# Kernel optimization log

Hardware: AMD Instinct MI355X
Metric: run time of the kernel (lower is better)

Reference implementation:

```python
import jax, jax.numpy as jnp
import numpy as np

HIDDEN = 4096
N_HEADS = 32
N_KV_HEADS = 8
HEAD_DIM = 128
ROPE_BASE = 10000.0


def setup_inputs() -> dict:
    key = jax.random.key(0)
    k1, k2, k3, k4, k5 = jax.random.split(key, 5)
    s = 0.02  # init scale for weights
    return {
        "hidden_states": jax.random.normal(k1, (1, 2048, HIDDEN), dtype=jnp.float32),
        "Wq": jax.random.normal(k2, (N_HEADS * HEAD_DIM, HIDDEN), dtype=jnp.float32) * s,
        "Wk": jax.random.normal(k3, (N_KV_HEADS * HEAD_DIM, HIDDEN), dtype=jnp.float32) * s,
        "Wv": jax.random.normal(k4, (N_KV_HEADS * HEAD_DIM, HIDDEN), dtype=jnp.float32) * s,
        "Wo": jax.random.normal(k5, (HIDDEN, HIDDEN), dtype=jnp.float32) * s,
    }


def _rope(x, cos, sin):
    # x: [B, H, T, D]; cos/sin: [T, D/2] -> rotate split halves (Llama style)
    d2 = x.shape[-1] // 2
    x1, x2 = x[..., :d2], x[..., d2:]
    return jnp.concatenate([x1 * cos - x2 * sin, x1 * sin + x2 * cos], axis=-1)


def reference(hidden_states, Wq, Wk, Wv, Wo):
    B, T, _ = hidden_states.shape
    H, Hkv, D = N_HEADS, N_KV_HEADS, HEAD_DIM
    G = H // Hkv  # kv groups

    q = jnp.einsum("bth,qh->btq", hidden_states, Wq).reshape(B, T, H, D).transpose(0, 2, 1, 3)
    k = jnp.einsum("bth,kh->btk", hidden_states, Wk).reshape(B, T, Hkv, D).transpose(0, 2, 1, 3)
    v = jnp.einsum("bth,vh->btv", hidden_states, Wv).reshape(B, T, Hkv, D).transpose(0, 2, 1, 3)

    # RoPE (position_offset = 0)
    positions = jnp.arange(T, dtype=jnp.float32)
    inv_freq = ROPE_BASE ** (-jnp.arange(0, D, 2, dtype=jnp.float32) / D)  # [D/2]
    angles = positions[:, None] * inv_freq[None, :]                        # [T, D/2]
    cos, sin = jnp.cos(angles), jnp.sin(angles)
    q = _rope(q, cos, sin)
    k = _rope(k, cos, sin)

    # GQA attention without materializing expanded K/V: group query heads
    qg = q.reshape(B, Hkv, G, T, D)
    scale = 1.0 / jnp.sqrt(jnp.asarray(D, dtype=q.dtype))
    scores = jnp.einsum("bkgtd,bksd->bkgts", qg, k) * scale  # [B, Hkv, G, T, T]
    causal = jnp.tril(jnp.ones((T, T), dtype=bool))
    scores = jnp.where(causal, scores, jnp.finfo(scores.dtype).min)
    probs = jax.nn.softmax(scores, axis=-1)
    attn = jnp.einsum("bkgts,bksd->bkgtd", probs, v)          # [B, Hkv, G, T, D]
    attn = attn.reshape(B, H, T, D).transpose(0, 2, 1, 3).reshape(B, T, H * D)

    return jnp.einsum("btq,oq->bto", attn, Wo)
```

## Files before the change

kernel.cpp:

```cpp
#include <hip/hip_runtime.h>
#include <stdint.h>

#define T_SEQ   2048
#define HID     4096
#define NH      32
#define NKV     8
#define HD      128
#define QCOLS   6144
#define QK_SCALE 0.08838834764831845f

typedef _Float16 half_t;
typedef _Float16 half8 __attribute__((ext_vector_type(8)));
typedef _Float16 half4v __attribute__((ext_vector_type(4)));
typedef float    f32x4 __attribute__((ext_vector_type(4)));

typedef __attribute__((address_space(1))) const void cg_void;
typedef __attribute__((address_space(3))) void lds_void;

__global__ __launch_bounds__(256) void cast_x_k(const float* __restrict__ X,
                                                half_t* __restrict__ Xh) {
  int i = blockIdx.x * 256 + threadIdx.x;
  f32x4 v = *(const f32x4*)(X + (size_t)i * 4);
  half4v o;
  o[0] = (half_t)v[0]; o[1] = (half_t)v[1]; o[2] = (half_t)v[2]; o[3] = (half_t)v[3];
  *(half4v*)(Xh + (size_t)i * 4) = o;
}

__global__ __launch_bounds__(256) void rope_tables_k(float* __restrict__ cs) {
  int idx = blockIdx.x * 256 + threadIdx.x;
  int t = idx >> 6, i = idx & 63;
  float inv = expf(-(float)i * 0.14391156831212787f);
  float a = (float)t * inv;
  cs[idx] = cosf(a);
  cs[131072 + idx] = sinf(a);
}

__global__ __launch_bounds__(256) void rope_vt_k(half_t* __restrict__ QKV,
                                                 const float* __restrict__ cs,
                                                 half_t* __restrict__ Vt) {
  if (blockIdx.x < 20480) {
    int idx = blockIdx.x * 256 + threadIdx.x;
    int i = idx & 63;
    int rem = idx >> 6;
    int head = rem % 40;
    int t = rem / 40;
    int colbase = (head < 32) ? head * HD : HID + (head - 32) * HD;
    size_t base = (size_t)t * QCOLS + colbase;
    float c = cs[t * 64 + i], s = cs[131072 + t * 64 + i];
    float x1 = (float)QKV[base + i];
    float x2 = (float)QKV[base + 64 + i];
    float o1 = x1 * c - x2 * s;
    float o2 = x1 * s + x2 * c;
    if (head < 32) { o1 *= QK_SCALE; o2 *= QK_SCALE; }
    QKV[base + i]      = (half_t)o1;
    QKV[base + 64 + i] = (half_t)o2;
  } else {
    int idx = (blockIdx.x - 20480) * 256 + threadIdx.x;
    int d  = idx & 127;
    int ts = (idx >> 7) & 255;
    int kh = idx >> 15;
    half8 o;
#pragma unroll
    for (int i = 0; i < 8; ++i)
      o[i] = QKV[(size_t)(ts * 8 + i) * QCOLS + HID + NKV * HD + kh * HD + d];
    *(half8*)&Vt[(size_t)kh * (HD * T_SEQ) + (size_t)d * T_SEQ + ts * 8] = o;
  }
}

template <int BM, int BN, int OUT_HALF>
__global__ __launch_bounds__(512, 2) void gemm8p_k(const half_t* __restrict__ A,
                                                   const float* __restrict__ Bq,
                                                   const float* __restrict__ Bk,
                                                   const float* __restrict__ Bv,
                                                   void* __restrict__ Cout,
                                                   int M, int N, int K) {
  constexpr int MF = BM / 32;
  constexpr int NF = BN / 64;
  constexpr int MH = MF / 2;
  constexpr int LA = BM / 64;
  constexpr int LB = BN / 64;
  __shared__ half_t Al[2][BM * 64];
  __shared__ half_t Bl[2][BN * 64];

  const int nbm = M / BM;
  const int nwg = nbm * (N / BN);
  const int bid = blockIdx.x;
  const int swz = (bid & 7) * (nwg >> 3) + (bid >> 3);
  const int brow = (swz % nbm) * BM;
  const int bcol = (swz / nbm) * BN;
  const int tid = threadIdx.x;
  const int lane = tid & 63, wid = tid >> 6;
  const int wr = wid >> 2, wc = wid & 3;
  const int lr = lane & 15, hi = lane >> 4;
  const int wrow = wr * (MF * 16), wcol = wc * (NF * 16);

  const half_t* Ab = A + (size_t)brow * K;

  const float* bp[LB];
#pragma unroll
  for (int l = 0; l < LB; ++l) {
    int c = l * 512 + tid, r = c >> 3, s = c & 7;
    int row = bcol + r;
    const float* src = (row < 4096) ? (Bq + (size_t)row * K)
                     : (row < 5120) ? (Bk + (size_t)(row - 4096) * K)
                                    : (Bv + (size_t)(row - 5120) * K);
    bp[l] = src + ((s ^ (r & 7)) * 8);
  }

  f32x4 acc[MF][NF] = {};
  half8 afr[MH], bfr[NF];
  f32x4 breg[LB][2];

#define STAGE_A(l, k0, buf) { \
    int c_ = (l) * 512 + tid; int r_ = c_ >> 3, s_ = c_ & 7; \
    __builtin_amdgcn_global_load_lds( \
      (cg_void*)(Ab + (size_t)r_ * K + (k0) + ((s_ ^ (r_ & 7)) * 8)), \
      (lds_void*)(&Al[buf][((l) * 512 + wid * 64) * 8]), 16, 0, 0); }
#define LOAD_B_ALL(k0) { \
    _Pragma("unroll") for (int l_ = 0; l_ < LB; ++l_) { \
      breg[l_][0] = *(const f32x4*)(bp[l_] + (k0)); \
      breg[l_][1] = *(const f32x4*)(bp[l_] + (k0) + 4); } }
#define WRITE_B_ALL(buf) { \
    _Pragma("unroll") for (int l_ = 0; l_ < LB; ++l_) { \
      half8 h_; \
      _Pragma("unroll") for (int e_ = 0; e_ < 4; ++e_) { \
        h_[e_] = (half_t)breg[l_][0][e_]; h_[4 + e_] = (half_t)breg[l_][1][e_]; } \
      *(half8*)&Bl[buf][((l_) * 512 + tid) * 8] = h_; } }
#define RD_A(i, mh, kk, buf) { \
    int row_ = wrow + ((mh) * MH + (i)) * 16 + lr; int ks_ = (kk) * 4 + hi; \
    afr[i] = *(const half8*)&Al[buf][row_ * 64 + ((ks_ ^ (row_ & 7)) * 8)]; }
#define RD_B(n, kk, buf) { \
    int row_ = wcol + (n) * 16 + lr; int ks_ = (kk) * 4 + hi; \
    bfr[n] = *(const half8*)&Bl[buf][row_ * 64 + ((ks_ ^ (row_ & 7)) * 8)]; }
#define MFMA_PH(mh) { \
    __builtin_amdgcn_s_setprio(1); \
    _Pragma("unroll") for (int i_ = 0; i_ < MH; ++i_) \
      _Pragma("unroll") for (int n_ = 0; n_ < NF; ++n_) \
        acc[(mh) * MH + i_][n_] = __builtin_amdgcn_mfma_f32_16x16x32_f16( \
            afr[i_], bfr[n_], acc[(mh) * MH + i_][n_], 0, 0, 0); \
    __builtin_amdgcn_s_setprio(0); }

#define DO_TILE(T, BUF) { \
    const int kn_ = ((T) + 1) * 64; const bool pf_ = ((T) + 1) < NT; \
    if (pf_) { _Pragma("unroll") for (int l_ = 0; l_ < LA; ++l_) STAGE_A(l_, kn_, (BUF) ^ 1); } \
    _Pragma("unroll") for (int n_ = 0; n_ < NF; ++n_) RD_B(n_, 0, BUF); \
    _Pragma("unroll") for (int i_ = 0; i_ < MH; ++i_) RD_A(i_, 0, 0, BUF); \
    MFMA_PH(0); \
    __builtin_amdgcn_s_barrier(); __builtin_amdgcn_sched_barrier(0); \
    if (pf_) { LOAD_B_ALL(kn_); } \
    _Pragma("unroll") for (int i_ = 0; i_ < MH; ++i_) RD_A(i_, 1, 0, BUF); \
    MFMA_PH(1); \
    __builtin_amdgcn_s_barrier(); __builtin_amdgcn_sched_barrier(0); \
    _Pragma("unroll") for (int n_ = 0; n_ < NF; ++n_) RD_B(n_, 1, BUF); \
    _Pragma("unroll") for (int i_ = 0; i_ < MH; ++i_) RD_A(i_, 1, 1, BUF); \
    MFMA_PH(1); \
    __builtin_amdgcn_s_barrier(); __builtin_amdgcn_sched_barrier(0); \
    _Pragma("unroll") for (int i_ = 0; i_ < MH; ++i_) RD_A(i_, 0, 1, BUF); \
    MFMA_PH(0); \
    if (pf_) { WRITE_B_ALL((BUF) ^ 1); } \
    asm volatile("s_waitcnt vmcnt(0)" ::: "memory"); \
    __syncthreads(); }

  const int NT = K / 64;
#pragma unroll
  for (int l_ = 0; l_ < LA; ++l_) STAGE_A(l_, 0, 0);
  LOAD_B_ALL(0);
  WRITE_B_ALL(0);
  asm volatile("s_waitcnt vmcnt(0)" ::: "memory");
  __syncthreads();

  for (int t = 0; t < NT; t += 2) {
    DO_TILE(t, 0);
    DO_TILE(t + 1, 1);
  }

#undef STAGE_A
#undef LOAD_B_ALL
#undef WRITE_B_ALL
#undef RD_A
#undef RD_B
#undef MFMA_PH
#undef DO_TILE

#pragma unroll
  for (int m = 0; m < MF; ++m)
#pragma unroll
    for (int n = 0; n < NF; ++n)
#pragma unroll
      for (int r = 0; r < 4; ++r) {
        int row = brow + wrow + m * 16 + hi * 4 + r;
        int col = bcol + wcol + n * 16 + lr;
        float v = acc[m][n][r];
        if (OUT_HALF) ((half_t*)Cout)[(size_t)row * N + col] = (half_t)v;
        else          ((float*)Cout)[(size_t)row * N + col] = v;
      }
}

__global__ __launch_bounds__(256, 2) void attn_k(const half_t* __restrict__ QKV,
                                                 const half_t* __restrict__ Vt,
                                                 half_t* __restrict__ Ob) {
  const int bid = blockIdx.x;
  const int qb = 31 - (bid >> 5);
  const int h  = bid & 31;
  const int kh = h >> 2;
  const int tid = threadIdx.x;
  const int lane = tid & 63;
  const int w = tid >> 6;
  const int lr = lane & 15, hi = lane >> 4;
  const int qrow = qb * 64 + w * 16;

  __shared__ half_t Klds[2][64 * 128];
  __shared__ half_t Vlds[2][128 * 64];
  __shared__ half_t Plds[4 * 16 * 72];

  const half_t* Qp  = QKV + h * HD;
  const half_t* Kp  = QKV + HID + kh * HD;
  const half_t* Vtp = Vt + (size_t)kh * (HD * T_SEQ);

  half8 qf[4];
#pragma unroll
  for (int kk = 0; kk < 4; ++kk)
    qf[kk] = *(const half8*)&Qp[(size_t)(qrow + lr) * QCOLS + kk * 32 + hi * 8];

  f32x4 acc[8] = {};
  float mrow[4], lrow[4];
#pragma unroll
  for (int r = 0; r < 4; ++r) { mrow[r] = -1e30f; lrow[r] = 0.0f; }

  half_t* Pw = &Plds[w * (16 * 72)];

#define STAGE_KV(kv0, buf) { \
    _Pragma("unroll") for (int c_ = 0; c_ < 4; ++c_) { \
      int chunk_ = c_ * 256 + tid; \
      int r_ = chunk_ >> 4, s_ = chunk_ & 15; \
      int cc_ = (s_ & 8) | ((s_ ^ r_) & 7); \
      __builtin_amdgcn_global_load_lds( \
          (cg_void*)(Kp + (size_t)((kv0) + r_) * QCOLS + cc_ * 8), \
          (lds_void*)(&Klds[buf][(c_ * 256 + w * 64) * 8]), 16, 0, 0); } \
    _Pragma("unroll") for (int c_ = 0; c_ < 4; ++c_) { \
      int chunk_ = c_ * 256 + tid; \
      int r_ = chunk_ >> 3, s_ = chunk_ & 7; \
      int cc_ = (s_ ^ r_) & 7; \
      __builtin_amdgcn_global_load_lds( \
          (cg_void*)(Vtp + (size_t)r_ * T_SEQ + (kv0) + cc_ * 8), \
          (lds_void*)(&Vlds[buf][(c_ * 256 + w * 64) * 8]), 16, 0, 0); } }

#define COMPUTE(T, BUF) { \
    const int kv0_ = (T) * 64; \
    f32x4 sc[4] = {}; \
    __builtin_amdgcn_s_setprio(1); \
    _Pragma("unroll") for (int jt_ = 0; jt_ < 4; ++jt_) \
      _Pragma("unroll") for (int kk_ = 0; kk_ < 4; ++kk_) { \
        int srow_ = jt_ * 16 + lr; \
        int sl_ = kk_ * 4 + hi; \
        int c_ = (sl_ & 8) | ((sl_ ^ srow_) & 7); \
        half8 kf_ = *(const half8*)&Klds[BUF][srow_ * 128 + c_ * 8]; \
        sc[jt_] = __builtin_amdgcn_mfma_f32_16x16x32_f16(qf[kk_], kf_, sc[jt_], 0, 0, 0); \
      } \
    __builtin_amdgcn_s_setprio(0); \
    if ((T) == qb) { \
      _Pragma("unroll") for (int jt_ = 0; jt_ < 4; ++jt_) \
        _Pragma("unroll") for (int r_ = 0; r_ < 4; ++r_) { \
          int ig_ = qrow + hi * 4 + r_; \
          int jg_ = kv0_ + jt_ * 16 + lr; \
          if (jg_ > ig_) sc[jt_][r_] = -1e30f; \
        } \
    } \
    float mx_[4]; \
    _Pragma("unroll") for (int r_ = 0; r_ < 4; ++r_) \
      mx_[r_] = fmaxf(fmaxf(sc[0][r_], sc[1][r_]), fmaxf(sc[2][r_], sc[3][r_])); \
    _Pragma("unroll") for (int off_ = 1; off_ < 16; off_ <<= 1) \
      _Pragma("unroll") for (int r_ = 0; r_ < 4; ++r_) \
        mx_[r_] = fmaxf(mx_[r_], __shfl_xor(mx_[r_], off_, 64)); \
    bool grow_ = false; \
    _Pragma("unroll") for (int r_ = 0; r_ < 4; ++r_) grow_ = grow_ || (mx_[r_] > mrow[r_] + 8.0f); \
    if (__any(grow_)) { \
      float scl_[4]; \
      _Pragma("unroll") for (int r_ = 0; r_ < 4; ++r_) { \
        float mn_ = fmaxf(mrow[r_], mx_[r_]); \
        scl_[r_] = __expf(mrow[r_] - mn_); \
        mrow[r_] = mn_; \
        float ls_ = 0.0f; \
        _Pragma("unroll") for (int jt_ = 0; jt_ < 4; ++jt_) { \
          sc[jt_][r_] = __expf(sc[jt_][r_] - mn_); ls_ += sc[jt_][r_]; } \
        lrow[r_] = lrow[r_] * scl_[r_] + ls_; \
      } \
      _Pragma("unroll") for (int g_ = 0; g_ < 8; ++g_) \
        _Pragma("unroll") for (int r_ = 0; r_ < 4; ++r_) acc[g_][r_] *= scl_[r_]; \
    } else { \
      _Pragma("unroll") for (int r_ = 0; r_ < 4; ++r_) { \
        float ls_ = 0.0f; \
        _Pragma("unroll") for (int jt_ = 0; jt_ < 4; ++jt_) { \
          sc[jt_][r_] = __expf(sc[jt_][r_] - mrow[r_]); ls_ += sc[jt_][r_]; } \
        lrow[r_] += ls_; \
      } \
    } \
    _Pragma("unroll") for (int jt_ = 0; jt_ < 4; ++jt_) \
      _Pragma("unroll") for (int r_ = 0; r_ < 4; ++r_) \
        Pw[(hi * 4 + r_) * 72 + jt_ * 16 + lr] = (half_t)sc[jt_][r_]; \
    half8 pf0_ = *(const half8*)&Pw[lr * 72 + hi * 8]; \
    half8 pf1_ = *(const half8*)&Pw[lr * 72 + 32 + hi * 8]; \
    __builtin_amdgcn_s_setprio(1); \
    _Pragma("unroll") for (int g_ = 0; g_ < 8; ++g_) { \
      int vrow_ = g_ * 16 + lr; \
      { int c0_ = (hi ^ vrow_) & 7; \
        half8 vf_ = *(const half8*)&Vlds[BUF][vrow_ * 64 + c0_ * 8]; \
        acc[g_] = __builtin_amdgcn_mfma_f32_16x16x32_f16(pf0_, vf_, acc[g_], 0, 0, 0); } \
      { int c1_ = ((4 + hi) ^ vrow_) & 7; \
        half8 vf_ = *(const half8*)&Vlds[BUF][vrow_ * 64 + c1_ * 8]; \
        acc[g_] = __builtin_amdgcn_mfma_f32_16x16x32_f16(pf1_, vf_, acc[g_], 0, 0, 0); } \
    } \
    __builtin_amdgcn_s_setprio(0); }

#define TILE_SYNC() { asm volatile("s_waitcnt vmcnt(0)" ::: "memory"); \
                      __builtin_amdgcn_s_barrier(); __builtin_amdgcn_sched_barrier(0); }

  const int nt = qb + 1;
  STAGE_KV(0, 0);
  TILE_SYNC();

  int t = 0;
  for (; t + 2 <= nt; t += 2) {
    STAGE_KV((t + 1) * 64, 1);
    COMPUTE(t, 0);
    TILE_SYNC();
    if (t + 2 < nt) { STAGE_KV((t + 2) * 64, 0); }
    COMPUTE(t + 1, 1);
    TILE_SYNC();
  }
  if (t < nt) { COMPUTE(t, 0); }

#undef STAGE_KV
#undef COMPUTE
#undef TILE_SYNC

  float linv[4];
#pragma unroll
  for (int r = 0; r < 4; ++r) {
    float l = lrow[r];
#pragma unroll
    for (int off = 1; off < 16; off <<= 1) l += __shfl_xor(l, off, 64);
    linv[r] = 1.0f / l;
  }
#pragma unroll
  for (int g = 0; g < 8; ++g)
#pragma unroll
    for (int r = 0; r < 4; ++r) {
      int row = qrow + hi * 4 + r;
      int col = h * HD + g * 16 + lr;
      Ob[(size_t)row * HID + col] = (half_t)(acc[g][r] * linv[r]);
    }
}

extern "C" void kernel_launch(void* const* d_in, const int* in_sizes, int n_in,
                              void* d_out, int out_size, void* d_ws, size_t ws_size,
                              hipStream_t stream) {
  const float* hs = (const float*)d_in[0];
  const float* Wq = (const float*)d_in[1];
  const float* Wk = (const float*)d_in[2];
  const float* Wv = (const float*)d_in[3];
  const float* Wo = (const float*)d_in[4];
  float* out = (float*)d_out;

  char* ws = (char*)d_ws;
  half_t* Xh    = (half_t*)(ws + 0);
  half_t* Vt    = (half_t*)(ws + 0);
  half_t* QKV   = (half_t*)(ws + 100663296);
  half_t* attnh = (half_t*)(ws + 125829120);
  float*  cs    = (float*)(ws + 142606336);
  if (ws_size < 143654912ull) return;

  cast_x_k<<<8192, 256, 0, stream>>>(hs, Xh);
  rope_tables_k<<<512, 256, 0, stream>>>(cs);

  gemm8p_k<256, 192, 1><<<256, 512, 0, stream>>>(Xh, Wq, Wk, Wv, (void*)QKV, 2048, 6144, 4096);
  rope_vt_k<<<21504, 256, 0, stream>>>(QKV, cs, Vt);
  attn_k<<<1024, 256, 0, stream>>>(QKV, Vt, attnh);
  gemm8p_k<256, 128, 0><<<256, 512, 0, stream>>>(attnh, Wo, Wo, Wo, (void*)out, 2048, 4096, 4096);
}
```

Baseline: 313.1 us.

## Transpose QK^T MFMA so P stays in registers, dropping LDS round-trip

Swaps the MFMA operands for the score computation so each lane holds one query row's scores, making row max/sum reductions need only two cross-lane shuffles instead of four per row. The P matrix is packed to fp16 with cvt_pkrtz and redistributed via ds_bpermute shuffles into the A-operand layout for the PV MFMA, removing the per-tile LDS write/read of P. This trades LDS traffic and shuffle reductions for extra permute shuffles and selects, and per-row rescale factors are broadcast across lanes.

```diff
diff --git a/kernel.cpp b/kernel.cpp
--- a/kernel.cpp
+++ b/kernel.cpp
@@ -12,10 +12,19 @@
 typedef _Float16 half_t;
 typedef _Float16 half8 __attribute__((ext_vector_type(8)));
 typedef _Float16 half4v __attribute__((ext_vector_type(4)));
+typedef __fp16   fp16x2 __attribute__((ext_vector_type(2)));
 typedef float    f32x4 __attribute__((ext_vector_type(4)));
 
 typedef __attribute__((address_space(1))) const void cg_void;
 typedef __attribute__((address_space(3))) void lds_void;
+
+typedef union { uint32_t u[4]; half8 h; } pfu;
+
+static __device__ __forceinline__ uint32_t pkrtz(float a, float b) {
+  union { fp16x2 h; uint32_t u; } c;
+  c.h = __builtin_amdgcn_cvt_pkrtz(a, b);
+  return c.u;
+}
 
 __global__ __launch_bounds__(256) void cast_x_k(const float* __restrict__ X,
                                                 half_t* __restrict__ Xh) {
@@ -211,7 +220,6 @@
 
   __shared__ half_t Klds[2][64 * 128];
   __shared__ half_t Vlds[2][128 * 64];
-  __shared__ half_t Plds[4 * 16 * 72];
 
   const half_t* Qp  = QKV + h * HD;
   const half_t* Kp  = QKV + HID + kh * HD;
@@ -223,11 +231,7 @@
     qf[kk] = *(const half8*)&Qp[(size_t)(qrow + lr) * QCOLS + kk * 32 + hi * 8];
 
   f32x4 acc[8] = {};
-  float mrow[4], lrow[4];
-#pragma unroll
-  for (int r = 0; r < 4; ++r) { mrow[r] = -1e30f; lrow[r] = 0.0f; }
-
-  half_t* Pw = &Plds[w * (16 * 72)];
+  float mrow = -1e30f, lrow = 0.0f;
 
 #define STAGE_KV(kv0, buf) { \
     _Pragma("unroll") for (int c_ = 0; c_ < 4; ++c_) { \
@@ -255,60 +259,79 @@
         int sl_ = kk_ * 4 + hi; \
         int c_ = (sl_ & 8) | ((sl_ ^ srow_) & 7); \
         half8 kf_ = *(const half8*)&Klds[BUF][srow_ * 128 + c_ * 8]; \
-        sc[jt_] = __builtin_amdgcn_mfma_f32_16x16x32_f16(qf[kk_], kf_, sc[jt_], 0, 0, 0); \
+        sc[jt_] = __builtin_amdgcn_mfma_f32_16x16x32_f16(kf_, qf[kk_], sc[jt_], 0, 0, 0); \
       } \
     __builtin_amdgcn_s_setprio(0); \
     if ((T) == qb) { \
+      int ig_ = qrow + lr; \
       _Pragma("unroll") for (int jt_ = 0; jt_ < 4; ++jt_) \
         _Pragma("unroll") for (int r_ = 0; r_ < 4; ++r_) { \
-          int ig_ = qrow + hi * 4 + r_; \
-          int jg_ = kv0_ + jt_ * 16 + lr; \
+          int jg_ = kv0_ + jt_ * 16 + hi * 4 + r_; \
           if (jg_ > ig_) sc[jt_][r_] = -1e30f; \
         } \
     } \
-    float mx_[4]; \
-    _Pragma("unroll") for (int r_ = 0; r_ < 4; ++r_) \
-      mx_[r_] = fmaxf(fmaxf(sc[0][r_], sc[1][r_]), fmaxf(sc[2][r_], sc[3][r_])); \
-    _Pragma("unroll") for (int off_ = 1; off_ < 16; off_ <<= 1) \
-      _Pragma("unroll") for (int r_ = 0; r_ < 4; ++r_) \
-        mx_[r_] = fmaxf(mx_[r_], __shfl_xor(mx_[r_], off_, 64)); \
-    bool grow_ = false; \
-    _Pragma("unroll") for (int r_ = 0; r_ < 4; ++r_) grow_ = grow_ || (mx_[r_] > mrow[r_] + 8.0f); \
-    if (__any(grow_)) { \
-      float scl_[4]; \
-      _Pragma("unroll") for (int r_ = 0; r_ < 4; ++r_) { \
-        float mn_ = fmaxf(mrow[r_], mx_[r_]); \
-        scl_[r_] = __expf(mrow[r_] - mn_); \
-        mrow[r_] = mn_; \
-        float ls_ = 0.0f; \
-        _Pragma("unroll") for (int jt_ = 0; jt_ < 4; ++jt_) { \
-          sc[jt_][r_] = __expf(sc[jt_][r_] - mn_); ls_ += sc[jt_][r_]; } \
-        lrow[r_] = lrow[r_] * scl_[r_] + ls_; \
-      } \
-      _Pragma("unroll") for (int g_ = 0; g_ < 8; ++g_) \
-        _Pragma("unroll") for (int r_ = 0; r_ < 4; ++r_) acc[g_][r_] *= scl_[r_]; \
-    } else { \
-      _Pragma("unroll") for (int r_ = 0; r_ < 4; ++r_) { \
-        float ls_ = 0.0f; \
-        _Pragma("unroll") for (int jt_ = 0; jt_ < 4; ++jt_) { \
-          sc[jt_][r_] = __expf(sc[jt_][r_] - mrow[r_]); ls_ += sc[jt_][r_]; } \
-        lrow[r_] += ls_; \
-      } \
-    } \
+    float pmax_ = sc[0][0]; \
     _Pragma("unroll") for (int jt_ = 0; jt_ < 4; ++jt_) \
       _Pragma("unroll") for (int r_ = 0; r_ < 4; ++r_) \
-        Pw[(hi * 4 + r_) * 72 + jt_ * 16 + lr] = (half_t)sc[jt_][r_]; \
-    half8 pf0_ = *(const half8*)&Pw[lr * 72 + hi * 8]; \
-    half8 pf1_ = *(const half8*)&Pw[lr * 72 + 32 + hi * 8]; \
+        pmax_ = fmaxf(pmax_, sc[jt_][r_]); \
+    pmax_ = fmaxf(pmax_, __shfl_xor(pmax_, 16, 64)); \
+    pmax_ = fmaxf(pmax_, __shfl_xor(pmax_, 32, 64)); \
+    if (__any(pmax_ > mrow + 8.0f)) { \
+      float mn_ = fmaxf(mrow, pmax_); \
+      float scl_ = __expf(mrow - mn_); \
+      mrow = mn_; \
+      float ls_ = 0.0f; \
+      _Pragma("unroll") for (int jt_ = 0; jt_ < 4; ++jt_) \
+        _Pragma("unroll") for (int r_ = 0; r_ < 4; ++r_) { \
+          sc[jt_][r_] = __expf(sc[jt_][r_] - mn_); ls_ += sc[jt_][r_]; } \
+      lrow = lrow * scl_ + ls_; \
+      float sclr_[4]; \
+      _Pragma("unroll") for (int r_ = 0; r_ < 4; ++r_) \
+        sclr_[r_] = __shfl(scl_, hi * 4 + r_, 16); \
+      _Pragma("unroll") for (int g_ = 0; g_ < 8; ++g_) \
+        _Pragma("unroll") for (int r_ = 0; r_ < 4; ++r_) acc[g_][r_] *= sclr_[r_]; \
+    } else { \
+      float ls_ = 0.0f; \
+      _Pragma("unroll") for (int jt_ = 0; jt_ < 4; ++jt_) \
+        _Pragma("unroll") for (int r_ = 0; r_ < 4; ++r_) { \
+          sc[jt_][r_] = __expf(sc[jt_][r_] - mrow); ls_ += sc[jt_][r_]; } \
+      lrow += ls_; \
+    } \
+     \
+    uint32_t pk_[4][2]; \
+    _Pragma("unroll") for (int jt_ = 0; jt_ < 4; ++jt_) { \
+      pk_[jt_][0] = pkrtz(sc[jt_][0], sc[jt_][1]); \
+      pk_[jt_][1] = pkrtz(sc[jt_][2], sc[jt_][3]); } \
+     \
+    const int s0_ = lr + ((hi & 1) << 5); \
+    const int s1_ = s0_ + 16; \
+    const bool hs_ = ((hi >> 1) & 1) != 0; \
+    pfu P0_, P1_; \
+    { uint32_t a_ = (uint32_t)__shfl((int)pk_[0][0], s0_, 64); \
+      uint32_t b_ = (uint32_t)__shfl((int)pk_[1][0], s0_, 64); P0_.u[0] = hs_ ? b_ : a_; } \
+    { uint32_t a_ = (uint32_t)__shfl((int)pk_[0][1], s0_, 64); \
+      uint32_t b_ = (uint32_t)__shfl((int)pk_[1][1], s0_, 64); P0_.u[1] = hs_ ? b_ : a_; } \
+    { uint32_t a_ = (uint32_t)__shfl((int)pk_[0][0], s1_, 64); \
+      uint32_t b_ = (uint32_t)__shfl((int)pk_[1][0], s1_, 64); P0_.u[2] = hs_ ? b_ : a_; } \
+    { uint32_t a_ = (uint32_t)__shfl((int)pk_[0][1], s1_, 64); \
+      uint32_t b_ = (uint32_t)__shfl((int)pk_[1][1], s1_, 64); P0_.u[3] = hs_ ? b_ : a_; } \
+    { uint32_t a_ = (uint32_t)__shfl((int)pk_[2][0], s0_, 64); \
+      uint32_t b_ = (uint32_t)__shfl((int)pk_[3][0], s0_, 64); P1_.u[0] = hs_ ? b_ : a_; } \
+    { uint32_t a_ = (uint32_t)__shfl((int)pk_[2][1], s0_, 64); \
+      uint32_t b_ = (uint32_t)__shfl((int)pk_[3][1], s0_, 64); P1_.u[1] = hs_ ? b_ : a_; } \
+    { uint32_t a_ = (uint32_t)__shfl((int)pk_[2][0], s1_, 64); \
+      uint32_t b_ = (uint32_t)__shfl((int)pk_[3][0], s1_, 64); P1_.u[2] = hs_ ? b_ : a_; } \
+    { uint32_t a_ = (uint32_t)__shfl((int)pk_[2][1], s1_, 64); \
+      uint32_t b_ = (uint32_t)__shfl((int)pk_[3][1], s1_, 64); P1_.u[3] = hs_ ? b_ : a_; } \
     __builtin_amdgcn_s_setprio(1); \
     _Pragma("unroll") for (int g_ = 0; g_ < 8; ++g_) { \
       int vrow_ = g_ * 16 + lr; \
       { int c0_ = (hi ^ vrow_) & 7; \
         half8 vf_ = *(const half8*)&Vlds[BUF][vrow_ * 64 + c0_ * 8]; \
-        acc[g_] = __builtin_amdgcn_mfma_f32_16x16x32_f16(pf0_, vf_, acc[g_], 0, 0, 0); } \
+        acc[g_] = __builtin_amdgcn_mfma_f32_16x16x32_f16(P0_.h, vf_, acc[g_], 0, 0, 0); } \
       { int c1_ = ((4 + hi) ^ vrow_) & 7; \
         half8 vf_ = *(const half8*)&Vlds[BUF][vrow_ * 64 + c1_ * 8]; \
-        acc[g_] = __builtin_amdgcn_mfma_f32_16x16x32_f16(pf1_, vf_, acc[g_], 0, 0, 0); } \
+        acc[g_] = __builtin_amdgcn_mfma_f32_16x16x32_f16(P1_.h, vf_, acc[g_], 0, 0, 0); } \
     } \
     __builtin_amdgcn_s_setprio(0); }
 
@@ -334,21 +357,20 @@
 #undef COMPUTE
 #undef TILE_SYNC
 
-  float linv[4];
-#pragma unroll
-  for (int r = 0; r < 4; ++r) {
-    float l = lrow[r];
-#pragma unroll
-    for (int off = 1; off < 16; off <<= 1) l += __shfl_xor(l, off, 64);
-    linv[r] = 1.0f / l;
-  }
+  float l = lrow;
+  l += __shfl_xor(l, 16, 64);
+  l += __shfl_xor(l, 32, 64);
+  float linv = 1.0f / l;
+  float linvr[4];
+#pragma unroll
+  for (int r = 0; r < 4; ++r) linvr[r] = __shfl(linv, hi * 4 + r, 16);
 #pragma unroll
   for (int g = 0; g < 8; ++g)
 #pragma unroll
     for (int r = 0; r < 4; ++r) {
       int row = qrow + hi * 4 + r;
       int col = h * HD + g * 16 + lr;
-      Ob[(size_t)row * HID + col] = (half_t)(acc[g][r] * linv[r]);
+      Ob[(size_t)row * HID + col] = (half_t)(acc[g][r] * linvr[r]);
     }
 }
 
```

Measured after the change: 304.7 us. 2.7% less time.
